# Performance work log

Measured on AMD Instinct MI355X. Metric: run time of the kernel, lower is better.

The kernel has to match this reference:

```python
import jax, jax.numpy as jnp
import numpy as np


def _procrustes_align(X, Y):
    """Batched similarity-transform (scipy-style Procrustes, reflection allowed).
    Aligns Y (pred) to X (target). X, Y: [B, N, 3]. Returns aligned Y: [B, N, 3].
    """
    muX = X.mean(axis=1, keepdims=True)                      # [B,1,3]
    muY = Y.mean(axis=1, keepdims=True)
    X0 = X - muX
    Y0 = Y - muY
    normX = jnp.sqrt((X0 ** 2).sum(axis=(1, 2), keepdims=True))  # [B,1,1]
    normY = jnp.sqrt((Y0 ** 2).sum(axis=(1, 2), keepdims=True))
    X0n = X0 / normX
    Y0n = Y0 / normY
    # 3x3 cross-covariance per batch element
    M = jnp.einsum('bni,bnj->bij', X0n, Y0n)                 # [B,3,3]
    U, s, Vt = jnp.linalg.svd(M)                             # batched tiny SVD
    # Optimal rotation Q = V @ U^T = (U @ Vt)^T  (minimizes ||Y0n @ Q - X0n||)
    Q = jnp.swapaxes(jnp.matmul(U, Vt), -1, -2)              # [B,3,3]
    traceTA = s.sum(-1)[:, None, None]                       # [B,1,1]
    Z = normX * traceTA * jnp.einsum('bni,bij->bnj', Y0n, Q) + muX
    return Z


def setup_inputs() -> dict:
    key = jax.random.key(0)
    k1, k2 = jax.random.split(key)
    B, N = 262144, 21
    pred_kp3d = jax.random.normal(k1, (B, N, 3), dtype=jnp.float32)
    target_kp3d = jax.random.normal(k2, (B, N, 3), dtype=jnp.float32)
    return {"pred_kp3d": pred_kp3d, "target_kp3d": target_kp3d}


def reference(pred_kp3d, target_kp3d):
    pred_aligned = _procrustes_align(target_kp3d, pred_kp3d)
    # mean per-joint Euclidean distance (PA-MPJPE style)
    err = jnp.sqrt(((pred_aligned - target_kp3d) ** 2).sum(-1)).mean()
    return err
```

## Files before the change

kernel.cpp:

```cpp
#include <hip/hip_runtime.h>
#include <math.h>

#define NPTS 21
#define FLB  63
#define BPW  16
#define WPB  4
#define BPB  (BPW * WPB)
#define THREADS (64 * WPB)
#define TVEC (BPW * FLB / 4)
#define FULLR (TVEC / 64)
#define TAILL (TVEC % 64)

__device__ __forceinline__ void async_cp16(const float* g, float* l) {
    __builtin_amdgcn_global_load_lds(
        (__attribute__((address_space(1))) void*)g,
        (__attribute__((address_space(3))) void*)l,
        16, 0, 0);
}

__global__ __launch_bounds__(THREADS, 5)
void pa_mpjpe(const float* __restrict__ pred,
              const float* __restrict__ targ,
              float* __restrict__ ws,
              int B)
{
    __shared__ __align__(16) float ly[WPB][BPW * FLB];
    __shared__ __align__(16) float lx[WPB][BPW * FLB];

    const int tid  = threadIdx.x;
    const int w    = tid >> 6;
    const int lane = tid & 63;
    const int b    = lane & (BPW - 1);
    const int sub  = lane >> 4;
    const int bw0  = blockIdx.x * BPB + w * BPW;

    {
        const float* gp = pred + (size_t)bw0 * FLB;
        const float* gt = targ + (size_t)bw0 * FLB;
        #pragma unroll
        for (int j = 0; j < FULLR; ++j)
            async_cp16(gp + 4 * (j * 64 + lane), &ly[w][4 * (j * 64)]);
        if (lane < TAILL)
            async_cp16(gp + 4 * (FULLR * 64 + lane), &ly[w][4 * (FULLR * 64)]);
        #pragma unroll
        for (int j = 0; j < FULLR; ++j)
            async_cp16(gt + 4 * (j * 64 + lane), &lx[w][4 * (j * 64)]);
        if (lane < TAILL)
            async_cp16(gt + 4 * (FULLR * 64 + lane), &lx[w][4 * (FULLR * 64)]);
    }
    __builtin_amdgcn_s_waitcnt(0x0F70);

    float py0[6], py1[6], py2[6];
    float sy0=0.f, sy1=0.f, sy2=0.f, syy=0.f;
    float sx0=0.f, sx1=0.f, sx2=0.f;
    float m00=0,m01=0,m02=0, m10=0,m11=0,m12=0, m20=0,m21=0,m22=0;
    const int base = b * FLB;
    #pragma unroll
    for (int k = 0; k < 6; ++k) {
        const int n = sub + 4 * k;
        if (n < NPTS) {
            const int o = base + 3 * n;
            float a = ly[w][o+0], e = ly[w][o+1], c = ly[w][o+2];
            float u = lx[w][o+0], v = lx[w][o+1], x2 = lx[w][o+2];
            py0[k] = a; py1[k] = e; py2[k] = c;
            sy0 += a; sy1 += e; sy2 += c;
            syy = fmaf(a, a, fmaf(e, e, fmaf(c, c, syy)));
            sx0 += u; sx1 += v; sx2 += x2;
            m00 = fmaf(u,a,m00); m01 = fmaf(u,e,m01); m02 = fmaf(u,c,m02);
            m10 = fmaf(v,a,m10); m11 = fmaf(v,e,m11); m12 = fmaf(v,c,m12);
            m20 = fmaf(x2,a,m20); m21 = fmaf(x2,e,m21); m22 = fmaf(x2,c,m22);
        } else {
            py0[k] = 0.f; py1[k] = 0.f; py2[k] = 0.f;
        }
    }

    #define COMB(v) { v += __shfl_xor(v, 16, 64); v += __shfl_xor(v, 32, 64); }
    COMB(sy0) COMB(sy1) COMB(sy2) COMB(syy)
    COMB(sx0) COMB(sx1) COMB(sx2)
    COMB(m00) COMB(m01) COMB(m02)
    COMB(m10) COMB(m11) COMB(m12)
    COMB(m20) COMB(m21) COMB(m22)
    #undef COMB

    const float invN = 1.0f / (float)NPTS;
    float mux0 = sx0*invN, mux1 = sx1*invN, mux2 = sx2*invN;
    float muy0 = sy0*invN, muy1 = sy1*invN, muy2 = sy2*invN;
    float ny2  = syy - (sy0*sy0 + sy1*sy1 + sy2*sy2) * invN;
    float c00 = m00 - sx0*sy0*invN, c01 = m01 - sx0*sy1*invN, c02 = m02 - sx0*sy2*invN;
    float c10 = m10 - sx1*sy0*invN, c11 = m11 - sx1*sy1*invN, c12 = m12 - sx1*sy2*invN;
    float c20 = m20 - sx2*sy0*invN, c21 = m21 - sx2*sy1*invN, c22 = m22 - sx2*sy2*invN;

    float q00=c00, q01=c10, q02=c20,
          q10=c01, q11=c11, q12=c21,
          q20=c02, q21=c12, q22=c22;
    #pragma unroll
    for (int it = 0; it < 6; ++it) {
        float C00 = q11*q22 - q12*q21;
        float C01 = q12*q20 - q10*q22;
        float C02 = q10*q21 - q11*q20;
        float C10 = q02*q21 - q01*q22;
        float C11 = q00*q22 - q02*q20;
        float C12 = q01*q20 - q00*q21;
        float C20 = q01*q12 - q02*q11;
        float C21 = q02*q10 - q00*q12;
        float C22 = q00*q11 - q01*q10;
        float det = q00*C00 + q01*C01 + q02*C02;
        float ad  = fmaxf(fabsf(det), 1e-30f);
        float sdet = copysignf(ad, det);
        float g  = __expf(0.333333333f * __logf(ad));
        float ha = 0.5f / g;
        float hb = 0.5f * g / sdet;
        q00 = ha*q00 + hb*C00; q01 = ha*q01 + hb*C01; q02 = ha*q02 + hb*C02;
        q10 = ha*q10 + hb*C10; q11 = ha*q11 + hb*C11; q12 = ha*q12 + hb*C12;
        q20 = ha*q20 + hb*C20; q21 = ha*q21 + hb*C21; q22 = ha*q22 + hb*C22;
    }

    float trP = q00*c00 + q01*c10 + q02*c20
              + q10*c01 + q11*c11 + q12*c21
              + q20*c02 + q21*c12 + q22*c22;
    float kk = trP / ny2;
    float r00=kk*q00, r01=kk*q01, r02=kk*q02;
    float r10=kk*q10, r11=kk*q11, r12=kk*q12;
    float r20=kk*q20, r21=kk*q21, r22=kk*q22;

    float errsum = 0.0f;
    #pragma unroll
    for (int k = 0; k < 6; ++k) {
        const int n = sub + 4 * k;
        if (n < NPTS) {
            const int o = base + 3 * n;
            float xa = lx[w][o+0], xb = lx[w][o+1], xc = lx[w][o+2];
            float u = py0[k] - muy0, v = py1[k] - muy1, x2 = py2[k] - muy2;
            float z0 = fmaf(u, r00, fmaf(v, r10, fmaf(x2, r20, mux0))) - xa;
            float z1 = fmaf(u, r01, fmaf(v, r11, fmaf(x2, r21, mux1))) - xb;
            float z2 = fmaf(u, r02, fmaf(v, r12, fmaf(x2, r22, mux2))) - xc;
            errsum += sqrtf(fmaf(z0, z0, fmaf(z1, z1, z2*z2)));
        }
    }

    #pragma unroll
    for (int off = 32; off > 0; off >>= 1) errsum += __shfl_down(errsum, off, 64);
    if (lane == 0) ws[blockIdx.x * WPB + w] = errsum;
}

__global__ __launch_bounds__(256)
void pa_reduce(const float* __restrict__ ws, float* __restrict__ out,
               int nblk, float inv_total)
{
    __shared__ float sw[4];
    float s = 0.0f;
    const float4* w4 = (const float4*)ws;
    const int n4 = nblk >> 2;
    for (int i = threadIdx.x; i < n4; i += 256) {
        float4 v = w4[i];
        s += (v.x + v.y) + (v.z + v.w);
    }
    #pragma unroll
    for (int off = 32; off > 0; off >>= 1) s += __shfl_down(s, off, 64);
    if ((threadIdx.x & 63) == 0) sw[threadIdx.x >> 6] = s;
    __syncthreads();
    if (threadIdx.x == 0)
        out[0] = (sw[0] + sw[1] + sw[2] + sw[3]) * inv_total;
}

extern "C" void kernel_launch(void* const* d_in, const int* in_sizes, int n_in,
                              void* d_out, int out_size, void* d_ws, size_t ws_size,
                              hipStream_t stream)
{
    const float* pred = (const float*)d_in[0];
    const float* targ = (const float*)d_in[1];
    float* out = (float*)d_out;
    float* ws  = (float*)d_ws;

    int B = in_sizes[0] / FLB;
    int grid = (B + BPB - 1) / BPB;
    int npart = grid * WPB;
    float inv_total = 1.0f / ((float)B * (float)NPTS);

    pa_mpjpe<<<grid, THREADS, 0, stream>>>(pred, targ, ws, B);
    pa_reduce<<<1, 256, 0, stream>>>(ws, out, npart, inv_total);
}
```

Measured before the change: 149.0 us.

## Use single-wave blocks with 32 batch elements split across two lanes each

Each block becomes a single 64-thread wavefront handling 32 batch elements, with two lanes per element instead of four. This halves the cross-lane shuffle reductions and doubles the batch work per lane, so the per-element 3x3 polar iteration is shared by fewer redundant lanes. It also changes block count, LDS footprint per block and occupancy hints. The cost is more registers and a longer serial loop per lane.

```diff
diff --git a/kernel.cpp b/kernel.cpp
--- a/kernel.cpp
+++ b/kernel.cpp
@@ -3,13 +3,12 @@
 
 #define NPTS 21
 #define FLB  63
-#define BPW  16
-#define WPB  4
-#define BPB  (BPW * WPB)
-#define THREADS (64 * WPB)
+#define BPW  32
+#define THREADS 64
 #define TVEC (BPW * FLB / 4)
 #define FULLR (TVEC / 64)
 #define TAILL (TVEC % 64)
+#define KMAX 11
 
 __device__ __forceinline__ void async_cp16(const float* g, float* l) {
     __builtin_amdgcn_global_load_lds(
@@ -18,50 +17,48 @@
         16, 0, 0);
 }
 
-__global__ __launch_bounds__(THREADS, 5)
+__global__ __launch_bounds__(THREADS, 3)
 void pa_mpjpe(const float* __restrict__ pred,
               const float* __restrict__ targ,
               float* __restrict__ ws,
               int B)
 {
-    __shared__ __align__(16) float ly[WPB][BPW * FLB];
-    __shared__ __align__(16) float lx[WPB][BPW * FLB];
+    __shared__ __align__(16) float ly[BPW * FLB];
+    __shared__ __align__(16) float lx[BPW * FLB];
 
-    const int tid  = threadIdx.x;
-    const int w    = tid >> 6;
-    const int lane = tid & 63;
+    const int lane = threadIdx.x & 63;
     const int b    = lane & (BPW - 1);
-    const int sub  = lane >> 4;
-    const int bw0  = blockIdx.x * BPB + w * BPW;
+    const int sub  = (lane >> 5) & 1;
+    const int b0   = blockIdx.x * BPW;
 
     {
-        const float* gp = pred + (size_t)bw0 * FLB;
-        const float* gt = targ + (size_t)bw0 * FLB;
+        const float* gp = pred + (size_t)b0 * FLB;
+        const float* gt = targ + (size_t)b0 * FLB;
         #pragma unroll
         for (int j = 0; j < FULLR; ++j)
-            async_cp16(gp + 4 * (j * 64 + lane), &ly[w][4 * (j * 64)]);
+            async_cp16(gp + 4 * (j * 64 + lane), ly + 4 * (j * 64));
         if (lane < TAILL)
-            async_cp16(gp + 4 * (FULLR * 64 + lane), &ly[w][4 * (FULLR * 64)]);
+            async_cp16(gp + 4 * (FULLR * 64 + lane), ly + 4 * (FULLR * 64));
         #pragma unroll
         for (int j = 0; j < FULLR; ++j)
-            async_cp16(gt + 4 * (j * 64 + lane), &lx[w][4 * (j * 64)]);
+            async_cp16(gt + 4 * (j * 64 + lane), lx + 4 * (j * 64));
         if (lane < TAILL)
-            async_cp16(gt + 4 * (FULLR * 64 + lane), &lx[w][4 * (FULLR * 64)]);
+            async_cp16(gt + 4 * (FULLR * 64 + lane), lx + 4 * (FULLR * 64));
     }
     __builtin_amdgcn_s_waitcnt(0x0F70);
 
-    float py0[6], py1[6], py2[6];
+    float py0[KMAX], py1[KMAX], py2[KMAX];
     float sy0=0.f, sy1=0.f, sy2=0.f, syy=0.f;
     float sx0=0.f, sx1=0.f, sx2=0.f;
     float m00=0,m01=0,m02=0, m10=0,m11=0,m12=0, m20=0,m21=0,m22=0;
     const int base = b * FLB;
     #pragma unroll
-    for (int k = 0; k < 6; ++k) {
-        const int n = sub + 4 * k;
+    for (int k = 0; k < KMAX; ++k) {
+        const int n = 2 * k + sub;
         if (n < NPTS) {
             const int o = base + 3 * n;
-            float a = ly[w][o+0], e = ly[w][o+1], c = ly[w][o+2];
-            float u = lx[w][o+0], v = lx[w][o+1], x2 = lx[w][o+2];
+            float a = ly[o+0], e = ly[o+1], c = ly[o+2];
+            float u = lx[o+0], v = lx[o+1], x2 = lx[o+2];
             py0[k] = a; py1[k] = e; py2[k] = c;
             sy0 += a; sy1 += e; sy2 += c;
             syy = fmaf(a, a, fmaf(e, e, fmaf(c, c, syy)));
@@ -74,7 +71,7 @@
         }
     }
 
-    #define COMB(v) { v += __shfl_xor(v, 16, 64); v += __shfl_xor(v, 32, 64); }
+    #define COMB(v) { v += __shfl_xor(v, 32, 64); }
     COMB(sy0) COMB(sy1) COMB(sy2) COMB(syy)
     COMB(sx0) COMB(sx1) COMB(sx2)
     COMB(m00) COMB(m01) COMB(m02)
@@ -125,11 +122,11 @@
 
     float errsum = 0.0f;
     #pragma unroll
-    for (int k = 0; k < 6; ++k) {
-        const int n = sub + 4 * k;
+    for (int k = 0; k < KMAX; ++k) {
+        const int n = 2 * k + sub;
         if (n < NPTS) {
             const int o = base + 3 * n;
-            float xa = lx[w][o+0], xb = lx[w][o+1], xc = lx[w][o+2];
+            float xa = lx[o+0], xb = lx[o+1], xc = lx[o+2];
             float u = py0[k] - muy0, v = py1[k] - muy1, x2 = py2[k] - muy2;
             float z0 = fmaf(u, r00, fmaf(v, r10, fmaf(x2, r20, mux0))) - xa;
             float z1 = fmaf(u, r01, fmaf(v, r11, fmaf(x2, r21, mux1))) - xb;
@@ -140,7 +137,7 @@
 
     #pragma unroll
     for (int off = 32; off > 0; off >>= 1) errsum += __shfl_down(errsum, off, 64);
-    if (lane == 0) ws[blockIdx.x * WPB + w] = errsum;
+    if (lane == 0) ws[blockIdx.x] = errsum;
 }
 
 __global__ __launch_bounds__(256)
@@ -173,10 +170,9 @@
     float* ws  = (float*)d_ws;
 
     int B = in_sizes[0] / FLB;
-    int grid = (B + BPB - 1) / BPB;
-    int npart = grid * WPB;
+    int grid = (B + BPW - 1) / BPW;
     float inv_total = 1.0f / ((float)B * (float)NPTS);
 
     pa_mpjpe<<<grid, THREADS, 0, stream>>>(pred, targ, ws, B);
-    pa_reduce<<<1, 256, 0, stream>>>(ws, out, npart, inv_total);
+    pa_reduce<<<1, 256, 0, stream>>>(ws, out, grid, inv_total);
 }
```

Result: no change. 146.7 us (-1.5%).
